# Optimization experiments

Measured on AMD Instinct MI355X. Metric: run time of the kernel, lower is better.

## Reference

```python
import jax, jax.numpy as jnp
import numpy as np

PANELTY_K = 0.055
HANNING_WINDOW_WEIGHT = 0.42
HANNING_WINDOW_SIZE_FACTOR = 2.0
PI = 3.141592653589793

N = 8192
NP = 2000  # proposals per roi


def _rois_vals(r):
    # r: (..., 4) as x1,y1,x2,y2
    x = (r[..., 0] + r[..., 2]) / 2.0
    y = (r[..., 1] + r[..., 3]) / 2.0
    w = jnp.abs(r[..., 0] - r[..., 2]) + 0.0001
    h = jnp.abs(r[..., 1] - r[..., 3]) + 0.0001
    p = (w + h) / 2.0
    s = jnp.sqrt((w + p) * (h + p))
    ratio = w / h
    return x, y, s, ratio


def setup_inputs() -> dict:
    key = jax.random.key(0)
    k1, k2, k3 = jax.random.split(key, 3)
    rois = jax.random.uniform(k1, (N, 4), dtype=jnp.float32)
    rpn_rois = jax.random.uniform(k2, (N, NP, 5), dtype=jnp.float32)
    scores = jax.random.uniform(k3, (N, NP, 2), dtype=jnp.float32)
    return {"rois": rois, "rpn_rois": rpn_rois, "scores": scores}


def reference(rois, rpn_rois, scores):
    # reference roi stats, broadcast over proposals: (N, 1)
    x, y, s, r = _rois_vals(rois[:, None, :])
    # proposal stats: (N, n)
    x_, y_, s_, r_ = _rois_vals(rpn_rois[:, :, 1:5])

    s_max = jnp.maximum(s / s_, s_ / s)
    r_max = jnp.maximum(r, 1.0 / r)  # faithful to source (uses ref ratio only)
    penalty_score = jnp.exp(-PANELTY_K * (s_max * r_max - 1.0))

    window_sz = s * HANNING_WINDOW_SIZE_FACTOR
    dist = jnp.sqrt((x - x_) ** 2 + (y - y_) ** 2)
    hanning = 0.5 + 0.5 * jnp.cos(dist * PI / window_sz)
    hanning = jnp.where(dist > window_sz, 0.0, hanning)

    penalty_window = scores[:, :, 1] * penalty_score + hanning * HANNING_WINDOW_WEIGHT
    inds = jnp.argmax(penalty_window, axis=1)  # (N,)

    sel_rpn_rois = jnp.take_along_axis(rpn_rois, inds[:, None, None], axis=1)[:, 0, 1:]   # (N, 4)
    sel_scores = jnp.take_along_axis(scores, inds[:, None, None], axis=1)[:, 0, 1:]       # (N, 1)
    return sel_rpn_rois, sel_scores
```

## Files before the change

### kernel.cpp

```cpp
#include <hip/hip_runtime.h>
#include <math.h>

#define NPROP 2000
#define RPN_ROW (NPROP * 5)
#define SC_ROW  (NPROP * 2)
#define PANELTY_K 0.055f
#define HANN_W 0.42f
#define PI_F 3.14159265358979323846f

typedef float f4 __attribute__((ext_vector_type(4)));

__global__ __launch_bounds__(256) void trnms_kernel(
    const float* __restrict__ rois,
    const float* __restrict__ rpn,
    const float* __restrict__ scores,
    float* __restrict__ out_rois,
    float* __restrict__ out_scores)
{
    const int i   = blockIdx.x;
    const int tid = threadIdx.x;

    const float rx1 = rois[i * 4 + 0], ry1 = rois[i * 4 + 1];
    const float rx2 = rois[i * 4 + 2], ry2 = rois[i * 4 + 3];
    const float x = (rx1 + rx2) * 0.5f;
    const float y = (ry1 + ry2) * 0.5f;
    const float w = fabsf(rx1 - rx2) + 0.0001f;
    const float h = fabsf(ry1 - ry2) + 0.0001f;
    const float p = (w + h) * 0.5f;
    const float s = sqrtf((w + p) * (h + p));
    const float ratio = w / h;
    const float r_max = fmaxf(ratio, 1.0f / ratio);
    const float window = s * 2.0f;

    const float* __restrict__ rowr  = rpn    + (long long)i * RPN_ROW;
    const float* __restrict__ rowsc = scores + (long long)i * SC_ROW;
    const f4* __restrict__ rowr4  = (const f4*)rowr;
    const f4* __restrict__ rowsc4 = (const f4*)rowsc;

    float best  = -INFINITY;
    int   besti = 0x7fffffff;

    auto eval = [&](float px1, float py1, float px2, float py2, float scj, int j) {
        const float x_ = (px1 + px2) * 0.5f;
        const float y_ = (py1 + py2) * 0.5f;
        const float w_ = fabsf(px1 - px2) + 0.0001f;
        const float h_ = fabsf(py1 - py2) + 0.0001f;
        const float p_ = (w_ + h_) * 0.5f;
        const float s_ = sqrtf((w_ + p_) * (h_ + p_));
        const float smax = fmaxf(s / s_, s_ / s);
        const float pen  = expf(-PANELTY_K * (smax * r_max - 1.0f));
        const float dx = x - x_;
        const float dy = y - y_;
        const float dist = sqrtf(dx * dx + dy * dy);
        float han = 0.5f + 0.5f * cosf(dist * PI_F / window);
        han = (dist > window) ? 0.0f : han;
        const float val = scj * pen + han * HANN_W;
        if (val > best) { best = val; besti = j; }
    };

    #pragma unroll
    for (int c = 0; c < 2; ++c) {
        const int t4 = c * 256 + tid;
        const int j0 = t4 * 4;
        if (j0 < NPROP) {
            const f4 v0 = rowr4[t4 * 5 + 0];
            const f4 v1 = rowr4[t4 * 5 + 1];
            const f4 v2 = rowr4[t4 * 5 + 2];
            const f4 v3 = rowr4[t4 * 5 + 3];
            const f4 v4 = rowr4[t4 * 5 + 4];
            const f4 s0 = rowsc4[t4 * 2 + 0];
            const f4 s1 = rowsc4[t4 * 2 + 1];

            eval(v0.y, v0.z, v0.w, v1.x, s0.y, j0 + 0);
            eval(v1.z, v1.w, v2.x, v2.y, s0.w, j0 + 1);
            eval(v2.w, v3.x, v3.y, v3.z, s1.y, j0 + 2);
            eval(v4.x, v4.y, v4.z, v4.w, s1.w, j0 + 3);
        }
    }

    #pragma unroll
    for (int off = 32; off > 0; off >>= 1) {
        const float ov = __shfl_down(best, off);
        const int   oi = __shfl_down(besti, off);
        if (ov > best || (ov == best && oi < besti)) { best = ov; besti = oi; }
    }

    __shared__ float sval[4];
    __shared__ int   sidx[4];
    const int wave = tid >> 6;
    if ((tid & 63) == 0) { sval[wave] = best; sidx[wave] = besti; }
    __syncthreads();

    if (tid == 0) {
        #pragma unroll
        for (int k = 1; k < 4; ++k) {
            const float ov = sval[k];
            const int   oi = sidx[k];
            if (ov > best || (ov == best && oi < besti)) { best = ov; besti = oi; }
        }
        out_rois[i * 4 + 0] = rowr[besti * 5 + 1];
        out_rois[i * 4 + 1] = rowr[besti * 5 + 2];
        out_rois[i * 4 + 2] = rowr[besti * 5 + 3];
        out_rois[i * 4 + 3] = rowr[besti * 5 + 4];
        out_scores[i] = rowsc[besti * 2 + 1];
    }
}

extern "C" void kernel_launch(void* const* d_in, const int* in_sizes, int n_in,
                              void* d_out, int out_size, void* d_ws, size_t ws_size,
                              hipStream_t stream) {
    const float* rois   = (const float*)d_in[0];
    const float* rpn    = (const float*)d_in[1];
    const float* scores = (const float*)d_in[2];

    const int N = in_sizes[0] / 4;

    float* out_rois   = (float*)d_out;
    float* out_scores = (float*)d_out + N * 4;

    trnms_kernel<<<N, 256, 0, stream>>>(rois, rpn, scores, out_rois, out_scores);
}
```

Before: 503.4 us.

## Stage proposal rows through swizzled LDS for coalesced global loads

Each half of a row's proposals and scores is now copied into shared memory with fully contiguous f4 loads, using an XOR swizzle on the LDS index. Threads then read their 5+2 strided f4 values from LDS instead of global memory. The goal is to avoid the stride-5 and stride-2 uncoalesced global access pattern. The cost is about 28KB of LDS per block, two extra barriers per chunk, and only 250 of 256 threads computing in each chunk, which can lower occupancy and remove overlap between loading and computing.

```diff
diff --git a/kernel.cpp b/kernel.cpp
--- a/kernel.cpp
+++ b/kernel.cpp
@@ -8,7 +8,15 @@
 #define HANN_W 0.42f
 #define PI_F 3.14159265358979323846f
 
+#define CHUNK   1000
+#define RPN_F4  (CHUNK * 5 / 4)
+#define SC_F4   (CHUNK * 2 / 4)
+#define STG_F4  (RPN_F4 + SC_F4)
+#define STG_PAD 1752
+
 typedef float f4 __attribute__((ext_vector_type(4)));
+
+__device__ __forceinline__ int swz(int idx) { return idx ^ ((idx >> 3) & 7); }
 
 __global__ __launch_bounds__(256) void trnms_kernel(
     const float* __restrict__ rois,
@@ -19,6 +27,10 @@
 {
     const int i   = blockIdx.x;
     const int tid = threadIdx.x;
+
+    __shared__ f4    stg[STG_PAD];
+    __shared__ float sval[4];
+    __shared__ int   sidx[4];
 
     const float rx1 = rois[i * 4 + 0], ry1 = rois[i * 4 + 1];
     const float rx2 = rois[i * 4 + 2], ry2 = rois[i * 4 + 3];
@@ -58,24 +70,33 @@
         if (val > best) { best = val; besti = j; }
     };
 
-    #pragma unroll
     for (int c = 0; c < 2; ++c) {
-        const int t4 = c * 256 + tid;
-        const int j0 = t4 * 4;
-        if (j0 < NPROP) {
-            const f4 v0 = rowr4[t4 * 5 + 0];
-            const f4 v1 = rowr4[t4 * 5 + 1];
-            const f4 v2 = rowr4[t4 * 5 + 2];
-            const f4 v3 = rowr4[t4 * 5 + 3];
-            const f4 v4 = rowr4[t4 * 5 + 4];
-            const f4 s0 = rowsc4[t4 * 2 + 0];
-            const f4 s1 = rowsc4[t4 * 2 + 1];
+        const f4* __restrict__ src_r = rowr4  + c * RPN_F4;
+        const f4* __restrict__ src_s = rowsc4 + c * SC_F4;
+        for (int k = tid; k < STG_F4; k += 256) {
+            const f4 v = (k < RPN_F4) ? src_r[k] : src_s[k - RPN_F4];
+            stg[swz(k)] = v;
+        }
+        __syncthreads();
+
+        if (tid < CHUNK / 4) {
+            const int g  = tid;
+            const int j0 = c * CHUNK + g * 4;
+            const int gb = g * 5;
+            const f4 v0 = stg[swz(gb + 0)];
+            const f4 v1 = stg[swz(gb + 1)];
+            const f4 v2 = stg[swz(gb + 2)];
+            const f4 v3 = stg[swz(gb + 3)];
+            const f4 v4 = stg[swz(gb + 4)];
+            const f4 s0 = stg[swz(RPN_F4 + g * 2 + 0)];
+            const f4 s1 = stg[swz(RPN_F4 + g * 2 + 1)];
 
             eval(v0.y, v0.z, v0.w, v1.x, s0.y, j0 + 0);
             eval(v1.z, v1.w, v2.x, v2.y, s0.w, j0 + 1);
             eval(v2.w, v3.x, v3.y, v3.z, s1.y, j0 + 2);
             eval(v4.x, v4.y, v4.z, v4.w, s1.w, j0 + 3);
         }
+        __syncthreads();
     }
 
     #pragma unroll
@@ -85,8 +106,6 @@
         if (ov > best || (ov == best && oi < besti)) { best = ov; besti = oi; }
     }
 
-    __shared__ float sval[4];
-    __shared__ int   sidx[4];
     const int wave = tid >> 6;
     if ((tid & 63) == 0) { sval[wave] = best; sidx[wave] = besti; }
     __syncthreads();
```

After: 514.0 us. +2.1%, slower.
